# Optimization experiments

Hardware: AMD Instinct MI355X
Metric: run time of the kernel (lower is better)

## Reference

```python
import jax, jax.numpy as jnp
import numpy as np

N_QUBITS = 4
DEPTH = 3
OUT_DIM = 256
BN_EPS = 1e-5


def _apply_ry(state, theta, q):
    # state: (B,2,2,2,2) complex64, theta: (B,) float32, gate on qubit q
    st = jnp.moveaxis(state, q + 1, -1)            # (B,2,2,2,2) with target last
    half = theta * 0.5
    c = jnp.cos(half)[:, None, None, None]
    s = jnp.sin(half)[:, None, None, None]
    a0, a1 = st[..., 0], st[..., 1]
    st = jnp.stack([c * a0 - s * a1, s * a0 + c * a1], axis=-1)
    return jnp.moveaxis(st, -1, q + 1)


def _apply_rz(state, theta, q):
    # theta: scalar (shared param). RZ = diag(e^{-i t/2}, e^{i t/2})
    st = jnp.moveaxis(state, q + 1, -1)
    p0 = jnp.exp(-0.5j * theta)
    p1 = jnp.exp(0.5j * theta)
    st = jnp.stack([st[..., 0] * p0, st[..., 1] * p1], axis=-1)
    return jnp.moveaxis(st, -1, q + 1)


def _apply_cnot(state, c, t):
    st = jnp.moveaxis(state, (c + 1, t + 1), (-2, -1))  # (...,2_c,2_t)
    st = jnp.stack([st[..., 0, :], st[..., 1, ::-1]], axis=-2)
    return jnp.moveaxis(st, (-2, -1), (c + 1, t + 1))


def _simulate(qparams, x):
    # Batched 4-qubit statevector sim. x: (B,4) data angles, qparams: (24,)
    B = x.shape[0]
    state = jnp.zeros((B, 16), jnp.complex64).at[:, 0].set(1.0)
    state = state.reshape(B, 2, 2, 2, 2)
    for d in range(DEPTH):
        for i in range(N_QUBITS):
            # RY(data) then RY(param) on same wire == RY(data+param)
            state = _apply_ry(state, x[:, i] + qparams[d * 2 * N_QUBITS + i], i)
        for i in range(N_QUBITS):
            state = _apply_cnot(state, i, (i + 1) % N_QUBITS)
        for i in range(N_QUBITS):
            theta = qparams[d * 2 * N_QUBITS + N_QUBITS + i]
            state = _apply_rz(state, jnp.broadcast_to(theta, ()), i)
    probs = jnp.abs(state) ** 2                      # (B,2,2,2,2) float32
    axes = (1, 2, 3, 4)
    z = []
    for i in range(N_QUBITS):
        p = probs.sum(axis=tuple(a for a in axes if a != i + 1))  # (B,2)
        z.append(p[:, 0] - p[:, 1])
    return jnp.stack(z, axis=1).astype(jnp.float32)  # (B,4) <Z_i>


def _batchnorm(h, g, b):
    m = h.mean(axis=0)
    v = h.var(axis=0)  # biased, as torch uses for normalization in train mode
    return (h - m) * jax.lax.rsqrt(v + BN_EPS) * g + b


def setup_inputs() -> dict:
    key = jax.random.key(0)
    ks = jax.random.split(key, 8)
    B = 65536
    x = jax.random.normal(ks[0], (B, N_QUBITS), jnp.float32)
    qparams = jax.random.normal(ks[1], (DEPTH * 2 * N_QUBITS,), jnp.float32)
    fc1_w = jax.random.normal(ks[2], (128, N_QUBITS), jnp.float32) * 0.3
    fc1_b = jnp.zeros((128,), jnp.float32)
    fc2_w = jax.random.normal(ks[3], (256, 128), jnp.float32) * 0.08
    fc2_b = jnp.zeros((256,), jnp.float32)
    fc3_w = jax.random.normal(ks[4], (OUT_DIM, 256), jnp.float32) * 0.06
    fc3_b = jnp.zeros((OUT_DIM,), jnp.float32)
    bn1_g = jnp.ones((128,), jnp.float32)
    bn1_b = jnp.zeros((128,), jnp.float32)
    bn2_g = jnp.ones((256,), jnp.float32)
    bn2_b = jnp.zeros((256,), jnp.float32)
    return dict(x=x, qparams=qparams, fc1_w=fc1_w, fc1_b=fc1_b,
                bn1_g=bn1_g, bn1_b=bn1_b, fc2_w=fc2_w, fc2_b=fc2_b,
                bn2_g=bn2_g, bn2_b=bn2_b, fc3_w=fc3_w, fc3_b=fc3_b)


def reference(x, qparams, fc1_w, fc1_b, bn1_g, bn1_b, fc2_w, fc2_b,
              bn2_g, bn2_b, fc3_w, fc3_b):
    q = _simulate(qparams, x)                              # (B,4)
    h = jax.nn.relu(_batchnorm(q @ fc1_w.T + fc1_b, bn1_g, bn1_b))
    h = jax.nn.relu(_batchnorm(h @ fc2_w.T + fc2_b, bn2_g, bn2_b))
    out = jnp.tanh(h @ fc3_w.T + fc3_b)                    # (B,256)
    return out.reshape(-1, 1, 16, 16)
```

## Files before the change

kernel.cpp:

```cpp
#include <hip/hip_runtime.h>

typedef __attribute__((ext_vector_type(8))) _Float16 f16x8;
typedef __attribute__((ext_vector_type(16))) float f32x16;

#define MFMA32(a, b, c) __builtin_amdgcn_mfma_f32_32x32x16_f16((a), (b), (c), 0, 0, 0)

__device__ __forceinline__ float tanh_fast(float x) {
  return 1.0f - 2.0f / (__expf(2.0f * x) + 1.0f);
}

__global__ __launch_bounds__(256) void k_quantum(
    const float4* __restrict__ x, const float* __restrict__ qp,
    float4* __restrict__ qout, float* __restrict__ stats, int QB,
    const float* __restrict__ w2, const float* __restrict__ w3,
    _Float16* __restrict__ w2f, _Float16* __restrict__ w3f)
{
  int tid = threadIdx.x;

  if (blockIdx.x >= QB) {
    int i = (blockIdx.x - QB) * 256 + tid;
    w3f[i] = (_Float16)w3[i];
    if (i < 32768) w2f[i] = (_Float16)w2[i];
    return;
  }

  size_t r = (size_t)blockIdx.x * 256 + tid;
  float4 xr = x[r];
  float xv[4] = {xr.x, xr.y, xr.z, xr.w};

  float re[16], im[16];
#pragma unroll
  for (int i = 0; i < 16; i++) { re[i] = 0.f; im[i] = 0.f; }
  re[0] = 1.f;

#pragma unroll
  for (int d = 0; d < 3; d++) {
#pragma unroll
    for (int q = 0; q < 4; q++) {
      float th = 0.5f * (xv[q] + qp[d * 8 + q]);
      float s, c; __sincosf(th, &s, &c);
      int m = 8 >> q;
#pragma unroll
      for (int i = 0; i < 16; i++) if (!(i & m)) {
        int i1 = i | m;
        float r0 = re[i], i0 = im[i], r1 = re[i1], i1v = im[i1];
        re[i]  = c * r0 - s * r1;  im[i]  = c * i0 - s * i1v;
        re[i1] = s * r0 + c * r1;  im[i1] = s * i0 + c * i1v;
      }
    }
#pragma unroll
    for (int q = 0; q < 4; q++) {
      int mc = 8 >> q, mt = 8 >> ((q + 1) & 3);
#pragma unroll
      for (int i = 0; i < 16; i++) if ((i & mc) && !(i & mt)) {
        int i1 = i | mt;
        float tr = re[i]; re[i] = re[i1]; re[i1] = tr;
        float ti = im[i]; im[i] = im[i1]; im[i1] = ti;
      }
    }
#pragma unroll
    for (int q = 0; q < 4; q++) {
      float th = 0.5f * qp[d * 8 + 4 + q];
      float s, c; __sincosf(th, &s, &c);
      int m = 8 >> q;
#pragma unroll
      for (int i = 0; i < 16; i++) {
        float pi = (i & m) ? s : -s;
        float r0 = re[i], i0 = im[i];
        re[i] = r0 * c - i0 * pi;
        im[i] = r0 * pi + i0 * c;
      }
    }
  }

  float p[16];
#pragma unroll
  for (int i = 0; i < 16; i++) p[i] = re[i] * re[i] + im[i] * im[i];
  float z[4];
#pragma unroll
  for (int q = 0; q < 4; q++) {
    int m = 8 >> q; float acc = 0.f;
#pragma unroll
    for (int i = 0; i < 16; i++) acc += (i & m) ? -p[i] : p[i];
    z[q] = acc;
  }
  qout[r] = make_float4(z[0], z[1], z[2], z[3]);

  float st[14];
  st[0] = z[0]; st[1] = z[1]; st[2] = z[2]; st[3] = z[3];
  int p5 = 4;
#pragma unroll
  for (int a = 0; a < 4; a++)
#pragma unroll
    for (int b = a; b < 4; b++) st[p5++] = z[a] * z[b];

  __shared__ float part[4][14];
  int lane = tid & 63, wv = tid >> 6;
#pragma unroll
  for (int s = 0; s < 14; s++) {
    float v = st[s];
#pragma unroll
    for (int o = 32; o; o >>= 1) v += __shfl_down(v, o, 64);
    if (lane == 0) part[wv][s] = v;
  }
  __syncthreads();
  if (tid < 14)
    atomicAdd(stats + tid, part[0][tid] + part[1][tid] + part[2][tid] + part[3][tid]);
}

__global__ void k_prep1(const float* __restrict__ w1, const float* __restrict__ b1,
                        const float* __restrict__ g, const float* __restrict__ bb,
                        const float* __restrict__ stats, float* __restrict__ w1e,
                        float* __restrict__ b1e, float invB)
{
  int j = threadIdx.x;
  float qb0 = stats[0] * invB, qb1 = stats[1] * invB, qb2 = stats[2] * invB, qb3 = stats[3] * invB;
  float M00 = stats[4] * invB, M01 = stats[5] * invB, M02 = stats[6] * invB, M03 = stats[7] * invB;
  float M11 = stats[8] * invB, M12 = stats[9] * invB, M13 = stats[10] * invB;
  float M22 = stats[11] * invB, M23 = stats[12] * invB, M33 = stats[13] * invB;
  float w0 = w1[j * 4 + 0], wv1 = w1[j * 4 + 1], wv2 = w1[j * 4 + 2], wv3 = w1[j * 4 + 3];
  float b = b1[j];
  float wq = w0 * qb0 + wv1 * qb1 + wv2 * qb2 + wv3 * qb3;
  float m = wq + b;
  float quad = w0 * w0 * M00 + wv1 * wv1 * M11 + wv2 * wv2 * M22 + wv3 * wv3 * M33
             + 2.f * (w0 * wv1 * M01 + w0 * wv2 * M02 + w0 * wv3 * M03
                    + wv1 * wv2 * M12 + wv1 * wv3 * M13 + wv2 * wv3 * M23);
  float e2 = quad + 2.f * b * wq + b * b;
  float var = e2 - m * m;
  float s = g[j] * rsqrtf(var + 1e-5f);
  w1e[j * 4 + 0] = s * w0; w1e[j * 4 + 1] = s * wv1;
  w1e[j * 4 + 2] = s * wv2; w1e[j * 4 + 3] = s * wv3;
  b1e[j] = s * b + bb[j] - s * m;
}

__global__ __launch_bounds__(256, 2) void k_fc2stats(
    const float4* __restrict__ q, const float4* __restrict__ w1e4,
    const float* __restrict__ b1e, const _Float16* __restrict__ w2f,
    const float* __restrict__ b2,
    float* __restrict__ s2sum, float* __restrict__ s2sq)
{
  __shared__ __align__(16) float4 qs[128];
  __shared__ __align__(16) _Float16 a1[128 * 136];

  int t = threadIdx.x;
  int lane = t & 63, w = t >> 6, m32 = lane & 31, hh = lane >> 5;
  size_t rowBase = (size_t)blockIdx.x * 128;

  if (t < 128) qs[t] = q[rowBase + t];
  __syncthreads();

  {
    int j = t & 127;
    float4 w1 = w1e4[j];
    float b1v = b1e[j];
    int rb = (t >> 7) * 64;
#pragma unroll 8
    for (int i = 0; i < 64; i++) {
      float4 qv = qs[rb + i];
      float v = fmaf(w1.x, qv.x, fmaf(w1.y, qv.y, fmaf(w1.z, qv.z, fmaf(w1.w, qv.w, b1v))));
      a1[(rb + i) * 136 + j] = (_Float16)fmaxf(v, 0.f);
    }
  }
  __syncthreads();

  f32x16 acc[4][2];
#pragma unroll
  for (int mt = 0; mt < 4; mt++)
#pragma unroll
    for (int nt = 0; nt < 2; nt++)
#pragma unroll
      for (int r = 0; r < 16; r++) acc[mt][nt][r] = 0.f;

#pragma unroll
  for (int ks = 0; ks < 8; ks++) {
    int kb = ks * 16 + hh * 8;
    f16x8 bfr[2];
#pragma unroll
    for (int nt = 0; nt < 2; nt++)
      bfr[nt] = *(const f16x8*)(w2f + (size_t)(w * 64 + nt * 32 + m32) * 128 + kb);
#pragma unroll
    for (int mt = 0; mt < 4; mt++) {
      f16x8 afr = *(const f16x8*)&a1[(mt * 32 + m32) * 136 + kb];
#pragma unroll
      for (int nt = 0; nt < 2; nt++)
        acc[mt][nt] = MFMA32(afr, bfr[nt], acc[mt][nt]);
    }
  }

#pragma unroll
  for (int nt = 0; nt < 2; nt++) {
    int col = w * 64 + nt * 32 + m32;
    float b2v = b2[col];
    float s = 0.f, ss = 0.f;
#pragma unroll
    for (int mt = 0; mt < 4; mt++)
#pragma unroll
      for (int r = 0; r < 16; r++) {
        float hv = acc[mt][nt][r] + b2v;
        s += hv; ss += hv * hv;
      }
    s += __shfl_down(s, 32, 64);
    ss += __shfl_down(ss, 32, 64);
    if (lane < 32) {
      atomicAdd(&s2sum[col], s);
      atomicAdd(&s2sq[col], ss);
    }
  }
}

__global__ void k_prep2(const float* __restrict__ g, const float* __restrict__ bb,
                        const float* __restrict__ b2,
                        const float* __restrict__ s2sum, const float* __restrict__ s2sq,
                        float* __restrict__ sc2, float* __restrict__ t2, float invB)
{
  int j = threadIdx.x;
  float m = s2sum[j] * invB;
  float v = s2sq[j] * invB - m * m;
  float s = g[j] * rsqrtf(v + 1e-5f);
  sc2[j] = s;
  t2[j] = bb[j] - m * s + b2[j] * s;
}

__global__ __launch_bounds__(256, 2) void k_final(
    const float4* __restrict__ q, const float4* __restrict__ w1e4,
    const float* __restrict__ b1e, const _Float16* __restrict__ w2f,
    const float* __restrict__ sc2, const float* __restrict__ t2g,
    const _Float16* __restrict__ w3f, const float* __restrict__ b3,
    float* __restrict__ out)
{
  __shared__ __align__(16) float4 qs[128];
  __shared__ __align__(16) _Float16 un[128 * 264];
  _Float16* a1 = un;
  _Float16* a2 = un;

  int t = threadIdx.x;
  int lane = t & 63, w = t >> 6, m32 = lane & 31, hh = lane >> 5;
  size_t rowBase = (size_t)blockIdx.x * 128;

  if (t < 128) qs[t] = q[rowBase + t];
  __syncthreads();

  {
    int j = t & 127;
    float4 w1 = w1e4[j];
    float b1v = b1e[j];
    int rb = (t >> 7) * 64;
#pragma unroll 8
    for (int i = 0; i < 64; i++) {
      float4 qv = qs[rb + i];
      float v = fmaf(w1.x, qv.x, fmaf(w1.y, qv.y, fmaf(w1.z, qv.z, fmaf(w1.w, qv.w, b1v))));
      a1[(rb + i) * 136 + j] = (_Float16)fmaxf(v, 0.f);
    }
  }
  __syncthreads();

  f32x16 acc[4][2];
#pragma unroll
  for (int mt = 0; mt < 4; mt++)
#pragma unroll
    for (int nt = 0; nt < 2; nt++)
#pragma unroll
      for (int r = 0; r < 16; r++) acc[mt][nt][r] = 0.f;

#pragma unroll
  for (int ks = 0; ks < 8; ks++) {
    int kb = ks * 16 + hh * 8;
    f16x8 bfr[2];
#pragma unroll
    for (int nt = 0; nt < 2; nt++)
      bfr[nt] = *(const f16x8*)(w2f + (size_t)(w * 64 + nt * 32 + m32) * 128 + kb);
#pragma unroll
    for (int mt = 0; mt < 4; mt++) {
      f16x8 afr = *(const f16x8*)&a1[(mt * 32 + m32) * 136 + kb];
#pragma unroll
      for (int nt = 0; nt < 2; nt++)
        acc[mt][nt] = MFMA32(afr, bfr[nt], acc[mt][nt]);
    }
  }
  __syncthreads();

#pragma unroll
  for (int nt = 0; nt < 2; nt++) {
    int col = w * 64 + nt * 32 + m32;
    float sv = sc2[col], tv = t2g[col];
#pragma unroll
    for (int mt = 0; mt < 4; mt++)
#pragma unroll
      for (int r = 0; r < 16; r++) {
        int row = mt * 32 + (r & 3) + 8 * (r >> 2) + 4 * hh;
        a2[row * 264 + col] = (_Float16)fmaxf(fmaf(acc[mt][nt][r], sv, tv), 0.f);
      }
  }
  __syncthreads();

  f32x16 acc3[4][2];
#pragma unroll
  for (int mt = 0; mt < 4; mt++)
#pragma unroll
    for (int nt = 0; nt < 2; nt++)
#pragma unroll
      for (int r = 0; r < 16; r++) acc3[mt][nt][r] = 0.f;

#pragma unroll
  for (int ks = 0; ks < 16; ks++) {
    int kb = ks * 16 + hh * 8;
    f16x8 bfr[2];
#pragma unroll
    for (int nt = 0; nt < 2; nt++)
      bfr[nt] = *(const f16x8*)(w3f + (size_t)(w * 64 + nt * 32 + m32) * 256 + kb);
#pragma unroll
    for (int mt = 0; mt < 4; mt++) {
      f16x8 afr = *(const f16x8*)&a2[(mt * 32 + m32) * 264 + kb];
#pragma unroll
      for (int nt = 0; nt < 2; nt++)
        acc3[mt][nt] = MFMA32(afr, bfr[nt], acc3[mt][nt]);
    }
  }

#pragma unroll
  for (int nt = 0; nt < 2; nt++) {
    int col = w * 64 + nt * 32 + m32;
    float b3v = b3[col];
#pragma unroll
    for (int mt = 0; mt < 4; mt++)
#pragma unroll
      for (int r = 0; r < 16; r++) {
        int row = mt * 32 + (r & 3) + 8 * (r >> 2) + 4 * hh;
        out[(rowBase + row) * 256 + col] = tanh_fast(acc3[mt][nt][r] + b3v);
      }
  }
}

extern "C" void kernel_launch(void* const* d_in, const int* in_sizes, int n_in,
                              void* d_out, int out_size, void* d_ws, size_t ws_size,
                              hipStream_t stream) {
  const float* x     = (const float*)d_in[0];
  const float* qp    = (const float*)d_in[1];
  const float* fc1_w = (const float*)d_in[2];
  const float* fc1_b = (const float*)d_in[3];
  const float* bn1_g = (const float*)d_in[4];
  const float* bn1_b = (const float*)d_in[5];
  const float* fc2_w = (const float*)d_in[6];
  const float* fc2_b = (const float*)d_in[7];
  const float* bn2_g = (const float*)d_in[8];
  const float* bn2_b = (const float*)d_in[9];
  const float* fc3_w = (const float*)d_in[10];
  const float* fc3_b = (const float*)d_in[11];
  float* out = (float*)d_out;
  float* ws  = (float*)d_ws;

  int B = in_sizes[0] / 4;
  int QB = B / 256;

  float* wq    = ws;
  float* s1    = ws + (size_t)4 * B;
  float* w1e   = s1 + 16;
  float* b1e   = w1e + 512;
  float* s2sum = b1e + 128;
  float* s2sq  = s2sum + 256;
  float* sc2   = s2sq + 256;
  float* t2    = sc2 + 256;
  _Float16* w2f = (_Float16*)(t2 + 256);
  _Float16* w3f = w2f + 32768;

  hipMemsetAsync((void*)s1, 0, (16 + 512 + 128 + 256 + 256) * sizeof(float), stream);

  float invB = 1.0f / (float)B;

  k_quantum<<<QB + 256, 256, 0, stream>>>((const float4*)x, qp, (float4*)wq, s1, QB,
                                          fc2_w, fc3_w, w2f, w3f);
  k_prep1<<<1, 128, 0, stream>>>(fc1_w, fc1_b, bn1_g, bn1_b, s1, w1e, b1e, invB);
  k_fc2stats<<<B / 128, 256, 0, stream>>>((const float4*)wq, (const float4*)w1e, b1e,
                                          w2f, fc2_b, s2sum, s2sq);
  k_prep2<<<1, 256, 0, stream>>>(bn2_g, bn2_b, fc2_b, s2sum, s2sq, sc2, t2, invB);
  k_final<<<B / 128, 256, 0, stream>>>((const float4*)wq, (const float4*)w1e, b1e,
                                       w2f, sc2, t2, w3f, fc3_b, out);
}
```

Before: 151.0 us.

## Fuse whole pipeline into one cooperative kernel with grid-wide batchnorm syncs

Adds a single cooperative kernel that runs the quantum simulation, fc1 with batchnorm folded in, fc2 with MFMA, and fc3 with tanh. Grid syncs stand in for the separate stats and prep launches. The fc2 accumulators stay in registers across the second grid sync, so fc2 is no longer recomputed in the final stage. It also removes several kernel launches and the global round trip of the quantum outputs. The cost is about 70KB of LDS per block and a grid size capped by co-residency; if the cooperative launch fails, the old five-kernel path runs instead.

```diff
diff --git a/kernel.cpp b/kernel.cpp
--- a/kernel.cpp
+++ b/kernel.cpp
@@ -1,4 +1,7 @@
 #include <hip/hip_runtime.h>
+#include <hip/hip_cooperative_groups.h>
+
+namespace cg = cooperative_groups;
 
 typedef __attribute__((ext_vector_type(8))) _Float16 f16x8;
 typedef __attribute__((ext_vector_type(16))) float f32x16;
@@ -8,6 +11,262 @@
 __device__ __forceinline__ float tanh_fast(float x) {
   return 1.0f - 2.0f / (__expf(2.0f * x) + 1.0f);
 }
+
+__global__ __launch_bounds__(256, 2) void k_fused(
+    const float4* __restrict__ x, const float* __restrict__ qp,
+    const float* __restrict__ w1, const float* __restrict__ b1,
+    const float* __restrict__ g1, const float* __restrict__ bb1,
+    const float* __restrict__ w2, const float* __restrict__ b2,
+    const float* __restrict__ g2, const float* __restrict__ bb2,
+    const float* __restrict__ w3, const float* __restrict__ b3,
+    float* __restrict__ out, float* __restrict__ s1,
+    float* __restrict__ s2sum, float* __restrict__ s2sq,
+    _Float16* __restrict__ w2f, _Float16* __restrict__ w3f, float invB)
+{
+  __shared__ __align__(16) float4 qs[128];
+  __shared__ __align__(16) _Float16 un[128 * 264];
+  __shared__ __align__(16) float4 w1e[128];
+  __shared__ float b1e[128];
+  __shared__ float sc2s[256];
+  __shared__ float t2s[256];
+  __shared__ float part[2][14];
+
+  int t = threadIdx.x;
+  int lane = t & 63, w = t >> 6, m32 = lane & 31, hh = lane >> 5;
+  size_t rowBase = (size_t)blockIdx.x * 128;
+  cg::grid_group grid = cg::this_grid();
+
+  if (t < 128) {
+    float4 xr = x[rowBase + t];
+    float xv[4] = {xr.x, xr.y, xr.z, xr.w};
+
+    float re[16], im[16];
+#pragma unroll
+    for (int i = 0; i < 16; i++) { re[i] = 0.f; im[i] = 0.f; }
+    re[0] = 1.f;
+
+#pragma unroll
+    for (int d = 0; d < 3; d++) {
+#pragma unroll
+      for (int q = 0; q < 4; q++) {
+        float th = 0.5f * (xv[q] + qp[d * 8 + q]);
+        float s, c; __sincosf(th, &s, &c);
+        int m = 8 >> q;
+#pragma unroll
+        for (int i = 0; i < 16; i++) if (!(i & m)) {
+          int i1 = i | m;
+          float r0 = re[i], i0 = im[i], r1 = re[i1], i1v = im[i1];
+          re[i]  = c * r0 - s * r1;  im[i]  = c * i0 - s * i1v;
+          re[i1] = s * r0 + c * r1;  im[i1] = s * i0 + c * i1v;
+        }
+      }
+#pragma unroll
+      for (int q = 0; q < 4; q++) {
+        int mc = 8 >> q, mt2 = 8 >> ((q + 1) & 3);
+#pragma unroll
+        for (int i = 0; i < 16; i++) if ((i & mc) && !(i & mt2)) {
+          int i1 = i | mt2;
+          float tr = re[i]; re[i] = re[i1]; re[i1] = tr;
+          float ti = im[i]; im[i] = im[i1]; im[i1] = ti;
+        }
+      }
+#pragma unroll
+      for (int q = 0; q < 4; q++) {
+        float th = 0.5f * qp[d * 8 + 4 + q];
+        float s, c; __sincosf(th, &s, &c);
+        int m = 8 >> q;
+#pragma unroll
+        for (int i = 0; i < 16; i++) {
+          float pi = (i & m) ? s : -s;
+          float r0 = re[i], i0 = im[i];
+          re[i] = r0 * c - i0 * pi;
+          im[i] = r0 * pi + i0 * c;
+        }
+      }
+    }
+
+    float p[16];
+#pragma unroll
+    for (int i = 0; i < 16; i++) p[i] = re[i] * re[i] + im[i] * im[i];
+    float z[4];
+#pragma unroll
+    for (int q = 0; q < 4; q++) {
+      int m = 8 >> q; float acc = 0.f;
+#pragma unroll
+      for (int i = 0; i < 16; i++) acc += (i & m) ? -p[i] : p[i];
+      z[q] = acc;
+    }
+    qs[t] = make_float4(z[0], z[1], z[2], z[3]);
+
+    float st[14];
+    st[0] = z[0]; st[1] = z[1]; st[2] = z[2]; st[3] = z[3];
+    int p5 = 4;
+#pragma unroll
+    for (int a = 0; a < 4; a++)
+#pragma unroll
+      for (int b = a; b < 4; b++) st[p5++] = z[a] * z[b];
+
+#pragma unroll
+    for (int s = 0; s < 14; s++) {
+      float v = st[s];
+#pragma unroll
+      for (int o = 32; o; o >>= 1) v += __shfl_down(v, o, 64);
+      if (lane == 0) part[w][s] = v;
+    }
+  } else {
+    int stride = gridDim.x * 128;
+    for (int i = blockIdx.x * 128 + (t - 128); i < 65536; i += stride) {
+      w3f[i] = (_Float16)w3[i];
+      if (i < 32768) w2f[i] = (_Float16)w2[i];
+    }
+  }
+  __syncthreads();
+  if (t < 14) atomicAdd(s1 + t, part[0][t] + part[1][t]);
+
+  grid.sync();
+
+  if (t < 128) {
+    int j = t;
+    float S0 = s1[0] * invB, S1 = s1[1] * invB, S2 = s1[2] * invB, S3 = s1[3] * invB;
+    float M00 = s1[4] * invB, M01 = s1[5] * invB, M02 = s1[6] * invB, M03 = s1[7] * invB;
+    float M11 = s1[8] * invB, M12 = s1[9] * invB, M13 = s1[10] * invB;
+    float M22 = s1[11] * invB, M23 = s1[12] * invB, M33 = s1[13] * invB;
+    float w0 = w1[j * 4 + 0], wv1 = w1[j * 4 + 1], wv2 = w1[j * 4 + 2], wv3 = w1[j * 4 + 3];
+    float b = b1[j];
+    float wq = w0 * S0 + wv1 * S1 + wv2 * S2 + wv3 * S3;
+    float mm = wq + b;
+    float quad = w0 * w0 * M00 + wv1 * wv1 * M11 + wv2 * wv2 * M22 + wv3 * wv3 * M33
+               + 2.f * (w0 * wv1 * M01 + w0 * wv2 * M02 + w0 * wv3 * M03
+                      + wv1 * wv2 * M12 + wv1 * wv3 * M13 + wv2 * wv3 * M23);
+    float e2 = quad + 2.f * b * wq + b * b;
+    float var = e2 - mm * mm;
+    float sv = g1[j] * rsqrtf(var + 1e-5f);
+    w1e[j] = make_float4(sv * w0, sv * wv1, sv * wv2, sv * wv3);
+    b1e[j] = sv * b + bb1[j] - sv * mm;
+  }
+  __syncthreads();
+
+  {
+    int j = t & 127;
+    float4 w1v = w1e[j];
+    float b1v = b1e[j];
+    int rb = (t >> 7) * 64;
+#pragma unroll 8
+    for (int i = 0; i < 64; i++) {
+      float4 qv = qs[rb + i];
+      float v = fmaf(w1v.x, qv.x, fmaf(w1v.y, qv.y, fmaf(w1v.z, qv.z, fmaf(w1v.w, qv.w, b1v))));
+      un[(rb + i) * 136 + j] = (_Float16)fmaxf(v, 0.f);
+    }
+  }
+  __syncthreads();
+
+  f32x16 acc[4][2];
+#pragma unroll
+  for (int mt = 0; mt < 4; mt++)
+#pragma unroll
+    for (int nt = 0; nt < 2; nt++)
+#pragma unroll
+      for (int r = 0; r < 16; r++) acc[mt][nt][r] = 0.f;
+
+#pragma unroll
+  for (int ks = 0; ks < 8; ks++) {
+    int kb = ks * 16 + hh * 8;
+    f16x8 bfr[2];
+#pragma unroll
+    for (int nt = 0; nt < 2; nt++)
+      bfr[nt] = *(const f16x8*)(w2f + (size_t)(w * 64 + nt * 32 + m32) * 128 + kb);
+#pragma unroll
+    for (int mt = 0; mt < 4; mt++) {
+      f16x8 afr = *(const f16x8*)&un[(mt * 32 + m32) * 136 + kb];
+#pragma unroll
+      for (int nt = 0; nt < 2; nt++)
+        acc[mt][nt] = MFMA32(afr, bfr[nt], acc[mt][nt]);
+    }
+  }
+
+#pragma unroll
+  for (int nt = 0; nt < 2; nt++) {
+    int col = w * 64 + nt * 32 + m32;
+    float b2v = b2[col];
+    float s = 0.f, ss = 0.f;
+#pragma unroll
+    for (int mt = 0; mt < 4; mt++)
+#pragma unroll
+      for (int r = 0; r < 16; r++) {
+        float hv = acc[mt][nt][r] + b2v;
+        s += hv; ss += hv * hv;
+      }
+    s += __shfl_down(s, 32, 64);
+    ss += __shfl_down(ss, 32, 64);
+    if (lane < 32) {
+      atomicAdd(&s2sum[col], s);
+      atomicAdd(&s2sq[col], ss);
+    }
+  }
+
+  grid.sync();
+
+  {
+    float mcol = s2sum[t] * invB;
+    float vcol = s2sq[t] * invB - mcol * mcol;
+    float sv = g2[t] * rsqrtf(vcol + 1e-5f);
+    sc2s[t] = sv;
+    t2s[t] = bb2[t] - mcol * sv + b2[t] * sv;
+  }
+  __syncthreads();
+
+#pragma unroll
+  for (int nt = 0; nt < 2; nt++) {
+    int col = w * 64 + nt * 32 + m32;
+    float sv = sc2s[col], tv = t2s[col];
+#pragma unroll
+    for (int mt = 0; mt < 4; mt++)
+#pragma unroll
+      for (int r = 0; r < 16; r++) {
+        int row = mt * 32 + (r & 3) + 8 * (r >> 2) + 4 * hh;
+        un[row * 264 + col] = (_Float16)fmaxf(fmaf(acc[mt][nt][r], sv, tv), 0.f);
+      }
+  }
+  __syncthreads();
+
+  f32x16 acc3[4][2];
+#pragma unroll
+  for (int mt = 0; mt < 4; mt++)
+#pragma unroll
+    for (int nt = 0; nt < 2; nt++)
+#pragma unroll
+      for (int r = 0; r < 16; r++) acc3[mt][nt][r] = 0.f;
+
+#pragma unroll
+  for (int ks = 0; ks < 16; ks++) {
+    int kb = ks * 16 + hh * 8;
+    f16x8 bfr[2];
+#pragma unroll
+    for (int nt = 0; nt < 2; nt++)
+      bfr[nt] = *(const f16x8*)(w3f + (size_t)(w * 64 + nt * 32 + m32) * 256 + kb);
+#pragma unroll
+    for (int mt = 0; mt < 4; mt++) {
+      f16x8 afr = *(const f16x8*)&un[(mt * 32 + m32) * 264 + kb];
+#pragma unroll
+      for (int nt = 0; nt < 2; nt++)
+        acc3[mt][nt] = MFMA32(afr, bfr[nt], acc3[mt][nt]);
+    }
+  }
+
+#pragma unroll
+  for (int nt = 0; nt < 2; nt++) {
+    int col = w * 64 + nt * 32 + m32;
+    float b3v = b3[col];
+#pragma unroll
+    for (int mt = 0; mt < 4; mt++)
+#pragma unroll
+      for (int r = 0; r < 16; r++) {
+        int row = mt * 32 + (r & 3) + 8 * (r >> 2) + 4 * hh;
+        out[(rowBase + row) * 256 + col] = tanh_fast(acc3[mt][nt][r] + b3v);
+      }
+  }
+}
+
 
 __global__ __launch_bounds__(256) void k_quantum(
     const float4* __restrict__ x, const float* __restrict__ qp,
@@ -334,7 +593,7 @@
 extern "C" void kernel_launch(void* const* d_in, const int* in_sizes, int n_in,
                               void* d_out, int out_size, void* d_ws, size_t ws_size,
                               hipStream_t stream) {
-  const float* x     = (const float*)d_in[0];
+  const float4* x    = (const float4*)d_in[0];
   const float* qp    = (const float*)d_in[1];
   const float* fc1_w = (const float*)d_in[2];
   const float* fc1_b = (const float*)d_in[3];
@@ -350,29 +609,51 @@
   float* ws  = (float*)d_ws;
 
   int B = in_sizes[0] / 4;
-  int QB = B / 256;
-
-  float* wq    = ws;
-  float* s1    = ws + (size_t)4 * B;
-  float* w1e   = s1 + 16;
-  float* b1e   = w1e + 512;
-  float* s2sum = b1e + 128;
-  float* s2sq  = s2sum + 256;
-  float* sc2   = s2sq + 256;
-  float* t2    = sc2 + 256;
-  _Float16* w2f = (_Float16*)(t2 + 256);
-  _Float16* w3f = w2f + 32768;
-
-  hipMemsetAsync((void*)s1, 0, (16 + 512 + 128 + 256 + 256) * sizeof(float), stream);
-
   float invB = 1.0f / (float)B;
 
-  k_quantum<<<QB + 256, 256, 0, stream>>>((const float4*)x, qp, (float4*)wq, s1, QB,
-                                          fc2_w, fc3_w, w2f, w3f);
-  k_prep1<<<1, 128, 0, stream>>>(fc1_w, fc1_b, bn1_g, bn1_b, s1, w1e, b1e, invB);
-  k_fc2stats<<<B / 128, 256, 0, stream>>>((const float4*)wq, (const float4*)w1e, b1e,
-                                          w2f, fc2_b, s2sum, s2sq);
-  k_prep2<<<1, 256, 0, stream>>>(bn2_g, bn2_b, fc2_b, s2sum, s2sq, sc2, t2, invB);
-  k_final<<<B / 128, 256, 0, stream>>>((const float4*)wq, (const float4*)w1e, b1e,
-                                       w2f, sc2, t2, w3f, fc3_b, out);
-}
+  {
+    float* s1    = ws;
+    float* s2sum = ws + 16;
+    float* s2sq  = ws + 272;
+    _Float16* w2f = (_Float16*)(ws + 528);
+    _Float16* w3f = w2f + 32768;
+
+    hipMemsetAsync((void*)ws, 0, 528 * sizeof(float), stream);
+
+    void* args[] = { (void*)&x, (void*)&qp, (void*)&fc1_w, (void*)&fc1_b,
+                     (void*)&bn1_g, (void*)&bn1_b, (void*)&fc2_w, (void*)&fc2_b,
+                     (void*)&bn2_g, (void*)&bn2_b, (void*)&fc3_w, (void*)&fc3_b,
+                     (void*)&out, (void*)&s1, (void*)&s2sum, (void*)&s2sq,
+                     (void*)&w2f, (void*)&w3f, (void*)&invB };
+    hipError_t err = hipLaunchCooperativeKernel((const void*)k_fused,
+                                                dim3(B / 128), dim3(256),
+                                                args, 0u, stream);
+    if (err == hipSuccess) return;
+    (void)hipGetLastError();
+  }
+
+  {
+    int QB = B / 256;
+    float* wq    = ws;
+    float* s1    = ws + (size_t)4 * B;
+    float* w1e   = s1 + 16;
+    float* b1e   = w1e + 512;
+    float* s2sum = b1e + 128;
+    float* s2sq  = s2sum + 256;
+    float* sc2   = s2sq + 256;
+    float* t2    = sc2 + 256;
+    _Float16* w2f = (_Float16*)(t2 + 256);
+    _Float16* w3f = w2f + 32768;
+
+    hipMemsetAsync((void*)s1, 0, (16 + 512 + 128 + 256 + 256) * sizeof(float), stream);
+
+    k_quantum<<<QB + 256, 256, 0, stream>>>(x, qp, (float4*)wq, s1, QB,
+                                            fc2_w, fc3_w, w2f, w3f);
+    k_prep1<<<1, 128, 0, stream>>>(fc1_w, fc1_b, bn1_g, bn1_b, s1, w1e, b1e, invB);
+    k_fc2stats<<<B / 128, 256, 0, stream>>>((const float4*)wq, (const float4*)w1e, b1e,
+                                            w2f, fc2_b, s2sum, s2sq);
+    k_prep2<<<1, 256, 0, stream>>>(bn2_g, bn2_b, fc2_b, s2sum, s2sq, sc2, t2, invB);
+    k_final<<<B / 128, 256, 0, stream>>>((const float4*)wq, (const float4*)w1e, b1e,
+                                         w2f, sc2, t2, w3f, fc3_b, out);
+  }
+}
```

New measurement: 235.0 us. 1.56x slower.

## Fold BN prep kernels and memset into consumer kernels, use per-block partial stats

Applied to the files above, without the earlier changes.

Removes the two single-block prep kernels and the memset, cutting the launch count from six operations to three. k_quantum now writes per-block partial stats instead of atomics and zeroes the fc2 stat accumulators. Every fc2/final block redundantly reduces the partials and recomputes the folded BN1 and BN2 coefficients into shared memory. This trades launch and serialization overhead for redundant per-block reduction work and extra shared memory, which may reduce occupancy.

```diff
diff --git a/kernel.cpp b/kernel.cpp
--- a/kernel.cpp
+++ b/kernel.cpp
@@ -11,16 +11,19 @@
 
 __global__ __launch_bounds__(256) void k_quantum(
     const float4* __restrict__ x, const float* __restrict__ qp,
-    float4* __restrict__ qout, float* __restrict__ stats, int QB,
+    float4* __restrict__ qout, float* __restrict__ s1part, int QB,
     const float* __restrict__ w2, const float* __restrict__ w3,
-    _Float16* __restrict__ w2f, _Float16* __restrict__ w3f)
+    _Float16* __restrict__ w2f, _Float16* __restrict__ w3f,
+    float* __restrict__ s2sum, float* __restrict__ s2sq)
 {
   int tid = threadIdx.x;
 
   if (blockIdx.x >= QB) {
-    int i = (blockIdx.x - QB) * 256 + tid;
+    int tb = blockIdx.x - QB;
+    int i = tb * 256 + tid;
     w3f[i] = (_Float16)w3[i];
     if (i < 32768) w2f[i] = (_Float16)w2[i];
+    if (tb == 0) { s2sum[tid] = 0.f; s2sq[tid] = 0.f; }
     return;
   }
 
@@ -105,59 +108,74 @@
   }
   __syncthreads();
   if (tid < 14)
-    atomicAdd(stats + tid, part[0][tid] + part[1][tid] + part[2][tid] + part[3][tid]);
+    s1part[blockIdx.x * 14 + tid] =
+        part[0][tid] + part[1][tid] + part[2][tid] + part[3][tid];
 }
 
-__global__ void k_prep1(const float* __restrict__ w1, const float* __restrict__ b1,
-                        const float* __restrict__ g, const float* __restrict__ bb,
-                        const float* __restrict__ stats, float* __restrict__ w1e,
-                        float* __restrict__ b1e, float invB)
-{
-  int j = threadIdx.x;
-  float qb0 = stats[0] * invB, qb1 = stats[1] * invB, qb2 = stats[2] * invB, qb3 = stats[3] * invB;
-  float M00 = stats[4] * invB, M01 = stats[5] * invB, M02 = stats[6] * invB, M03 = stats[7] * invB;
-  float M11 = stats[8] * invB, M12 = stats[9] * invB, M13 = stats[10] * invB;
-  float M22 = stats[11] * invB, M23 = stats[12] * invB, M33 = stats[13] * invB;
-  float w0 = w1[j * 4 + 0], wv1 = w1[j * 4 + 1], wv2 = w1[j * 4 + 2], wv3 = w1[j * 4 + 3];
-  float b = b1[j];
-  float wq = w0 * qb0 + wv1 * qb1 + wv2 * qb2 + wv3 * qb3;
-  float m = wq + b;
-  float quad = w0 * w0 * M00 + wv1 * wv1 * M11 + wv2 * wv2 * M22 + wv3 * wv3 * M33
-             + 2.f * (w0 * wv1 * M01 + w0 * wv2 * M02 + w0 * wv3 * M03
-                    + wv1 * wv2 * M12 + wv1 * wv3 * M13 + wv2 * wv3 * M23);
-  float e2 = quad + 2.f * b * wq + b * b;
-  float var = e2 - m * m;
-  float s = g[j] * rsqrtf(var + 1e-5f);
-  w1e[j * 4 + 0] = s * w0; w1e[j * 4 + 1] = s * wv1;
-  w1e[j * 4 + 2] = s * wv2; w1e[j * 4 + 3] = s * wv3;
-  b1e[j] = s * b + bb[j] - s * m;
-}
-
 __global__ __launch_bounds__(256, 2) void k_fc2stats(
-    const float4* __restrict__ q, const float4* __restrict__ w1e4,
-    const float* __restrict__ b1e, const _Float16* __restrict__ w2f,
-    const float* __restrict__ b2,
-    float* __restrict__ s2sum, float* __restrict__ s2sq)
+    const float4* __restrict__ q, const float* __restrict__ s1part, int QB,
+    const float* __restrict__ w1p, const float* __restrict__ b1p,
+    const float* __restrict__ g1p, const float* __restrict__ bb1p,
+    const _Float16* __restrict__ w2f, const float* __restrict__ b2,
+    float* __restrict__ s2sum, float* __restrict__ s2sq, float invB)
 {
   __shared__ __align__(16) float4 qs[128];
   __shared__ __align__(16) _Float16 a1[128 * 136];
+  __shared__ float r1[14][16];
+  __shared__ float s1v[14];
+  __shared__ __align__(16) float4 w1eS[128];
+  __shared__ float b1eS[128];
 
   int t = threadIdx.x;
   int lane = t & 63, w = t >> 6, m32 = lane & 31, hh = lane >> 5;
   size_t rowBase = (size_t)blockIdx.x * 128;
 
   if (t < 128) qs[t] = q[rowBase + t];
+  if (t < 224) {
+    int s = t >> 4, k = t & 15;
+    float acc = 0.f;
+    for (int j = k; j < QB; j += 16) acc += s1part[j * 14 + s];
+    r1[s][k] = acc;
+  }
+  __syncthreads();
+  if (t < 14) {
+    float v = 0.f;
+#pragma unroll
+    for (int k = 0; k < 16; k++) v += r1[t][k];
+    s1v[t] = v * invB;
+  }
+  __syncthreads();
+
+  if (t < 128) {
+    int j = t;
+    float S0 = s1v[0], S1 = s1v[1], S2 = s1v[2], S3 = s1v[3];
+    float M00 = s1v[4], M01 = s1v[5], M02 = s1v[6], M03 = s1v[7];
+    float M11 = s1v[8], M12 = s1v[9], M13 = s1v[10];
+    float M22 = s1v[11], M23 = s1v[12], M33 = s1v[13];
+    float w0 = w1p[j * 4 + 0], wv1 = w1p[j * 4 + 1], wv2 = w1p[j * 4 + 2], wv3 = w1p[j * 4 + 3];
+    float b = b1p[j];
+    float wq = w0 * S0 + wv1 * S1 + wv2 * S2 + wv3 * S3;
+    float mm = wq + b;
+    float quad = w0 * w0 * M00 + wv1 * wv1 * M11 + wv2 * wv2 * M22 + wv3 * wv3 * M33
+               + 2.f * (w0 * wv1 * M01 + w0 * wv2 * M02 + w0 * wv3 * M03
+                      + wv1 * wv2 * M12 + wv1 * wv3 * M13 + wv2 * wv3 * M23);
+    float e2 = quad + 2.f * b * wq + b * b;
+    float var = e2 - mm * mm;
+    float sv = g1p[j] * rsqrtf(var + 1e-5f);
+    w1eS[j] = make_float4(sv * w0, sv * wv1, sv * wv2, sv * wv3);
+    b1eS[j] = sv * b + bb1p[j] - sv * mm;
+  }
   __syncthreads();
 
   {
     int j = t & 127;
-    float4 w1 = w1e4[j];
-    float b1v = b1e[j];
+    float4 w1v = w1eS[j];
+    float b1v = b1eS[j];
     int rb = (t >> 7) * 64;
 #pragma unroll 8
     for (int i = 0; i < 64; i++) {
       float4 qv = qs[rb + i];
-      float v = fmaf(w1.x, qv.x, fmaf(w1.y, qv.y, fmaf(w1.z, qv.z, fmaf(w1.w, qv.w, b1v))));
+      float v = fmaf(w1v.x, qv.x, fmaf(w1v.y, qv.y, fmaf(w1v.z, qv.z, fmaf(w1v.w, qv.w, b1v))));
       a1[(rb + i) * 136 + j] = (_Float16)fmaxf(v, 0.f);
     }
   }
@@ -208,48 +226,83 @@
   }
 }
 
-__global__ void k_prep2(const float* __restrict__ g, const float* __restrict__ bb,
-                        const float* __restrict__ b2,
-                        const float* __restrict__ s2sum, const float* __restrict__ s2sq,
-                        float* __restrict__ sc2, float* __restrict__ t2, float invB)
-{
-  int j = threadIdx.x;
-  float m = s2sum[j] * invB;
-  float v = s2sq[j] * invB - m * m;
-  float s = g[j] * rsqrtf(v + 1e-5f);
-  sc2[j] = s;
-  t2[j] = bb[j] - m * s + b2[j] * s;
-}
-
 __global__ __launch_bounds__(256, 2) void k_final(
-    const float4* __restrict__ q, const float4* __restrict__ w1e4,
-    const float* __restrict__ b1e, const _Float16* __restrict__ w2f,
-    const float* __restrict__ sc2, const float* __restrict__ t2g,
+    const float4* __restrict__ q, const float* __restrict__ s1part, int QB,
+    const float* __restrict__ w1p, const float* __restrict__ b1p,
+    const float* __restrict__ g1p, const float* __restrict__ bb1p,
+    const _Float16* __restrict__ w2f, const float* __restrict__ b2,
+    const float* __restrict__ g2p, const float* __restrict__ bb2p,
+    const float* __restrict__ s2sum, const float* __restrict__ s2sq,
     const _Float16* __restrict__ w3f, const float* __restrict__ b3,
-    float* __restrict__ out)
+    float* __restrict__ out, float invB)
 {
   __shared__ __align__(16) float4 qs[128];
   __shared__ __align__(16) _Float16 un[128 * 264];
-  _Float16* a1 = un;
-  _Float16* a2 = un;
+  __shared__ float r1[14][16];
+  __shared__ float s1v[14];
+  __shared__ __align__(16) float4 w1eS[128];
+  __shared__ float b1eS[128];
+  __shared__ float sc2s[256];
+  __shared__ float t2s[256];
 
   int t = threadIdx.x;
   int lane = t & 63, w = t >> 6, m32 = lane & 31, hh = lane >> 5;
   size_t rowBase = (size_t)blockIdx.x * 128;
 
   if (t < 128) qs[t] = q[rowBase + t];
+  if (t < 224) {
+    int s = t >> 4, k = t & 15;
+    float acc = 0.f;
+    for (int j = k; j < QB; j += 16) acc += s1part[j * 14 + s];
+    r1[s][k] = acc;
+  }
+  {
+    float mcol = s2sum[t] * invB;
+    float vcol = s2sq[t] * invB - mcol * mcol;
+    float sv = g2p[t] * rsqrtf(vcol + 1e-5f);
+    sc2s[t] = sv;
+    t2s[t] = bb2p[t] - mcol * sv + b2[t] * sv;
+  }
+  __syncthreads();
+  if (t < 14) {
+    float v = 0.f;
+#pragma unroll
+    for (int k = 0; k < 16; k++) v += r1[t][k];
+    s1v[t] = v * invB;
+  }
+  __syncthreads();
+
+  if (t < 128) {
+    int j = t;
+    float S0 = s1v[0], S1 = s1v[1], S2 = s1v[2], S3 = s1v[3];
+    float M00 = s1v[4], M01 = s1v[5], M02 = s1v[6], M03 = s1v[7];
+    float M11 = s1v[8], M12 = s1v[9], M13 = s1v[10];
+    float M22 = s1v[11], M23 = s1v[12], M33 = s1v[13];
+    float w0 = w1p[j * 4 + 0], wv1 = w1p[j * 4 + 1], wv2 = w1p[j * 4 + 2], wv3 = w1p[j * 4 + 3];
+    float b = b1p[j];
+    float wq = w0 * S0 + wv1 * S1 + wv2 * S2 + wv3 * S3;
+    float mm = wq + b;
+    float quad = w0 * w0 * M00 + wv1 * wv1 * M11 + wv2 * wv2 * M22 + wv3 * wv3 * M33
+               + 2.f * (w0 * wv1 * M01 + w0 * wv2 * M02 + w0 * wv3 * M03
+                      + wv1 * wv2 * M12 + wv1 * wv3 * M13 + wv2 * wv3 * M23);
+    float e2 = quad + 2.f * b * wq + b * b;
+    float var = e2 - mm * mm;
+    float sv = g1p[j] * rsqrtf(var + 1e-5f);
+    w1eS[j] = make_float4(sv * w0, sv * wv1, sv * wv2, sv * wv3);
+    b1eS[j] = sv * b + bb1p[j] - sv * mm;
+  }
   __syncthreads();
 
   {
     int j = t & 127;
-    float4 w1 = w1e4[j];
-    float b1v = b1e[j];
+    float4 w1v = w1eS[j];
+    float b1v = b1eS[j];
     int rb = (t >> 7) * 64;
 #pragma unroll 8
     for (int i = 0; i < 64; i++) {
       float4 qv = qs[rb + i];
-      float v = fmaf(w1.x, qv.x, fmaf(w1.y, qv.y, fmaf(w1.z, qv.z, fmaf(w1.w, qv.w, b1v))));
-      a1[(rb + i) * 136 + j] = (_Float16)fmaxf(v, 0.f);
+      float v = fmaf(w1v.x, qv.x, fmaf(w1v.y, qv.y, fmaf(w1v.z, qv.z, fmaf(w1v.w, qv.w, b1v))));
+      un[(rb + i) * 136 + j] = (_Float16)fmaxf(v, 0.f);
     }
   }
   __syncthreads();
@@ -271,7 +324,7 @@
       bfr[nt] = *(const f16x8*)(w2f + (size_t)(w * 64 + nt * 32 + m32) * 128 + kb);
 #pragma unroll
     for (int mt = 0; mt < 4; mt++) {
-      f16x8 afr = *(const f16x8*)&a1[(mt * 32 + m32) * 136 + kb];
+      f16x8 afr = *(const f16x8*)&un[(mt * 32 + m32) * 136 + kb];
 #pragma unroll
       for (int nt = 0; nt < 2; nt++)
         acc[mt][nt] = MFMA32(afr, bfr[nt], acc[mt][nt]);
@@ -282,13 +335,13 @@
 #pragma unroll
   for (int nt = 0; nt < 2; nt++) {
     int col = w * 64 + nt * 32 + m32;
-    float sv = sc2[col], tv = t2g[col];
+    float sv = sc2s[col], tv = t2s[col];
 #pragma unroll
     for (int mt = 0; mt < 4; mt++)
 #pragma unroll
       for (int r = 0; r < 16; r++) {
         int row = mt * 32 + (r & 3) + 8 * (r >> 2) + 4 * hh;
-        a2[row * 264 + col] = (_Float16)fmaxf(fmaf(acc[mt][nt][r], sv, tv), 0.f);
+        un[row * 264 + col] = (_Float16)fmaxf(fmaf(acc[mt][nt][r], sv, tv), 0.f);
       }
   }
   __syncthreads();
@@ -310,7 +363,7 @@
       bfr[nt] = *(const f16x8*)(w3f + (size_t)(w * 64 + nt * 32 + m32) * 256 + kb);
 #pragma unroll
     for (int mt = 0; mt < 4; mt++) {
-      f16x8 afr = *(const f16x8*)&a2[(mt * 32 + m32) * 264 + kb];
+      f16x8 afr = *(const f16x8*)&un[(mt * 32 + m32) * 264 + kb];
 #pragma unroll
       for (int nt = 0; nt < 2; nt++)
         acc3[mt][nt] = MFMA32(afr, bfr[nt], acc3[mt][nt]);
@@ -351,28 +404,22 @@
 
   int B = in_sizes[0] / 4;
   int QB = B / 256;
-
-  float* wq    = ws;
-  float* s1    = ws + (size_t)4 * B;
-  float* w1e   = s1 + 16;
-  float* b1e   = w1e + 512;
-  float* s2sum = b1e + 128;
-  float* s2sq  = s2sum + 256;
-  float* sc2   = s2sq + 256;
-  float* t2    = sc2 + 256;
-  _Float16* w2f = (_Float16*)(t2 + 256);
+  float invB = 1.0f / (float)B;
+
+  float* wq     = ws;
+  float* s1part = ws + (size_t)4 * B;
+  float* s2sum  = s1part + (size_t)QB * 14;
+  float* s2sq   = s2sum + 256;
+  _Float16* w2f = (_Float16*)(s2sq + 256);
   _Float16* w3f = w2f + 32768;
 
-  hipMemsetAsync((void*)s1, 0, (16 + 512 + 128 + 256 + 256) * sizeof(float), stream);
-
-  float invB = 1.0f / (float)B;
-
-  k_quantum<<<QB + 256, 256, 0, stream>>>((const float4*)x, qp, (float4*)wq, s1, QB,
-                                          fc2_w, fc3_w, w2f, w3f);
-  k_prep1<<<1, 128, 0, stream>>>(fc1_w, fc1_b, bn1_g, bn1_b, s1, w1e, b1e, invB);
-  k_fc2stats<<<B / 128, 256, 0, stream>>>((const float4*)wq, (const float4*)w1e, b1e,
-                                          w2f, fc2_b, s2sum, s2sq);
-  k_prep2<<<1, 256, 0, stream>>>(bn2_g, bn2_b, fc2_b, s2sum, s2sq, sc2, t2, invB);
-  k_final<<<B / 128, 256, 0, stream>>>((const float4*)wq, (const float4*)w1e, b1e,
-                                       w2f, sc2, t2, w3f, fc3_b, out);
+  k_quantum<<<QB + 256, 256, 0, stream>>>((const float4*)x, qp, (float4*)wq, s1part, QB,
+                                          fc2_w, fc3_w, w2f, w3f, s2sum, s2sq);
+  k_fc2stats<<<B / 128, 256, 0, stream>>>((const float4*)wq, s1part, QB,
+                                          fc1_w, fc1_b, bn1_g, bn1_b,
+                                          w2f, fc2_b, s2sum, s2sq, invB);
+  k_final<<<B / 128, 256, 0, stream>>>((const float4*)wq, s1part, QB,
+                                       fc1_w, fc1_b, bn1_g, bn1_b,
+                                       w2f, fc2_b, bn2_g, bn2_b,
+                                       s2sum, s2sq, w3f, fc3_b, out, invB);
 }
```

Measured after the change: 146.4 us. 1.03x faster.
